# Optimization experiments

Measured on AMD Instinct MI355X. Metric: run time of the kernel, lower is better.

The kernel has to match this reference:

```python
import jax, jax.numpy as jnp
import numpy as np

B, S, D_IN, D_OUT = 4, 2048, 1024, 1024


def setup_inputs() -> dict:
    key = jax.random.key(0)
    ks = jax.random.split(key, 7)
    s_in = 1.0 / np.sqrt(D_IN)
    return {
        "x": jax.random.normal(ks[0], (B, S, D_IN), dtype=jnp.float32),
        "Wq": jax.random.uniform(ks[1], (D_IN, D_OUT), jnp.float32, -s_in, s_in),
        "bq": jax.random.uniform(ks[2], (D_OUT,), jnp.float32, -s_in, s_in),
        "Wk": jax.random.uniform(ks[3], (D_IN, D_OUT), jnp.float32, -s_in, s_in),
        "bk": jax.random.uniform(ks[4], (D_OUT,), jnp.float32, -s_in, s_in),
        "Wv": jax.random.uniform(ks[5], (D_IN, D_OUT), jnp.float32, -s_in, s_in),
        "bv": jax.random.uniform(ks[6], (D_OUT,), jnp.float32, -s_in, s_in),
    }


def reference(x, Wq, bq, Wk, bk, Wv, bv):
    # q,k,v: [B, S, D_OUT]
    q = jnp.einsum("bsd,de->bse", x, Wq) + bq
    k = jnp.einsum("bsd,de->bse", x, Wk) + bk
    v = jnp.einsum("bsd,de->bse", x, Wv) + bv
    scale = 1.0 / jnp.sqrt(jnp.asarray(q.shape[-1], q.dtype))
    scores = jnp.einsum("bqe,bke->bqk", q, k) * scale  # [B, S, S]
    attn = jax.nn.softmax(scores, axis=-1)
    return jnp.einsum("bqk,bke->bqe", attn, v)
```

## Files before the change

kernel.cpp:

```cpp
#include <hip/hip_runtime.h>
#include <hip/hip_bf16.h>
#include <stdint.h>


#define Bsz 4
#define Ssz 2048
#define Dsz 1024

typedef __attribute__((ext_vector_type(8))) short short8;
typedef __attribute__((ext_vector_type(4))) float floatx4;
typedef const __attribute__((address_space(1))) void* gptr_t;
typedef __attribute__((address_space(3))) void* lptr_t;

__device__ __forceinline__ ushort f32_to_bf16(float f) {
    union { float f; uint32_t u; } c; c.f = f;
    uint32_t u = c.u;
    u += 0x7fffu + ((u >> 16) & 1u);
    return (ushort)(u >> 16);
}

template <bool OUT_BF16>
__device__ __forceinline__ void gemm128(
    int bx, int by,
    const ushort* __restrict__ A, int lda,
    const ushort* __restrict__ Bt, int ldb,
    int K,
    void* __restrict__ Cout, int ldc,
    const float* __restrict__ bias, float alpha)
{
    __shared__ ushort lsA[2][128 * 32];
    __shared__ ushort lsB[2][128 * 32];

    const int tid  = threadIdx.x;
    const int row0 = by * 128;
    const int col0 = bx * 128;

    const int lane = tid & 63;
    const int wave = tid >> 6;
    const int wr   = (wave >> 1) * 64;
    const int wc   = (wave & 1) * 64;
    const int m16  = lane & 15;
    const int quad = lane >> 4;

    floatx4 acc[4][4];
#pragma unroll
    for (int i = 0; i < 4; i++)
#pragma unroll
        for (int j = 0; j < 4; j++) acc[i][j] = (floatx4){0.f, 0.f, 0.f, 0.f};

    const int srow = tid >> 2;
    const int skc  = (tid & 3) ^ ((srow >> 1) & 3);
    const ushort* ga = A  + (size_t)(row0 + srow) * lda + skc * 8;
    const ushort* gb = Bt + (size_t)(col0 + srow) * ldb + skc * 8;

    const int aoff = (quad ^ ((m16 >> 1) & 3)) * 8;

    __builtin_amdgcn_global_load_lds((gptr_t)(ga),                     (lptr_t)(lsA[0] + tid * 8),        16, 0, 0);
    __builtin_amdgcn_global_load_lds((gptr_t)(ga + (size_t)64 * lda), (lptr_t)(lsA[0] + 2048 + tid * 8), 16, 0, 0);
    __builtin_amdgcn_global_load_lds((gptr_t)(gb),                     (lptr_t)(lsB[0] + tid * 8),        16, 0, 0);
    __builtin_amdgcn_global_load_lds((gptr_t)(gb + (size_t)64 * ldb), (lptr_t)(lsB[0] + 2048 + tid * 8), 16, 0, 0);

    for (int k0 = 0; k0 < K; k0 += 32) {
        const int cur = (k0 >> 5) & 1;
        __syncthreads();
        if (k0 + 32 < K) {
            const int nxt = cur ^ 1;
            const int kn = k0 + 32;
            __builtin_amdgcn_global_load_lds((gptr_t)(ga + kn),                     (lptr_t)(lsA[nxt] + tid * 8),        16, 0, 0);
            __builtin_amdgcn_global_load_lds((gptr_t)(ga + kn + (size_t)64 * lda), (lptr_t)(lsA[nxt] + 2048 + tid * 8), 16, 0, 0);
            __builtin_amdgcn_global_load_lds((gptr_t)(gb + kn),                     (lptr_t)(lsB[nxt] + tid * 8),        16, 0, 0);
            __builtin_amdgcn_global_load_lds((gptr_t)(gb + kn + (size_t)64 * ldb), (lptr_t)(lsB[nxt] + 2048 + tid * 8), 16, 0, 0);
        }

        short8 af[4], bfr[4];
#pragma unroll
        for (int mi = 0; mi < 4; mi++)
            af[mi] = *(const short8*)&lsA[cur][(wr + mi * 16 + m16) * 32 + aoff];
#pragma unroll
        for (int ni = 0; ni < 4; ni++)
            bfr[ni] = *(const short8*)&lsB[cur][(wc + ni * 16 + m16) * 32 + aoff];
#pragma unroll
        for (int mi = 0; mi < 4; mi++)
#pragma unroll
            for (int ni = 0; ni < 4; ni++)
                acc[mi][ni] = __builtin_amdgcn_mfma_f32_16x16x32_bf16(af[mi], bfr[ni], acc[mi][ni], 0, 0, 0);
    }

#pragma unroll
    for (int ni = 0; ni < 4; ni++) {
        const int gcol = col0 + wc + ni * 16 + m16;
        const float bv = bias ? bias[gcol] : 0.0f;
#pragma unroll
        for (int mi = 0; mi < 4; mi++) {
            const int grow0 = row0 + wr + mi * 16 + quad * 4;
#pragma unroll
            for (int j = 0; j < 4; j++) {
                float v = (acc[mi][ni][j] + bv) * alpha;
                if (OUT_BF16)
                    ((ushort*)Cout)[(size_t)(grow0 + j) * ldc + gcol] = f32_to_bf16(v);
                else
                    ((float*)Cout)[(size_t)(grow0 + j) * ldc + gcol] = v;
            }
        }
    }
}

__global__ __launch_bounds__(256) void k_cvt_x(const float* __restrict__ x, ushort* __restrict__ xb) {
    int i = (blockIdx.x * 256 + threadIdx.x) * 4;
    float4 v = *(const float4*)(x + i);
    ushort4 o;
    o.x = f32_to_bf16(v.x); o.y = f32_to_bf16(v.y);
    o.z = f32_to_bf16(v.z); o.w = f32_to_bf16(v.w);
    *(ushort4*)(xb + i) = o;
}

__global__ __launch_bounds__(256) void k_wt(const float* __restrict__ Wq, const float* __restrict__ Wk,
                                            const float* __restrict__ Wv, ushort* __restrict__ Wt) {
    __shared__ float tile[32][33];
    const int z = blockIdx.z;
    const float* W = (z == 0) ? Wq : ((z == 1) ? Wk : Wv);
    ushort* out = Wt + (size_t)z * Dsz * Dsz;
    const int kb = blockIdx.y * 32, nb = blockIdx.x * 32;
    const int tx = threadIdx.x, ty = threadIdx.y;
#pragma unroll
    for (int j = 0; j < 32; j += 8)
        tile[ty + j][tx] = W[(size_t)(kb + ty + j) * Dsz + nb + tx];
    __syncthreads();
#pragma unroll
    for (int j = 0; j < 32; j += 8)
        out[(size_t)(nb + ty + j) * Dsz + kb + tx] = f32_to_bf16(tile[tx][ty + j]);
}

__global__ __launch_bounds__(256) void k_qkv(const ushort* __restrict__ xb, const ushort* __restrict__ Wt,
                                             const float* __restrict__ bq, const float* __restrict__ bk,
                                             const float* __restrict__ bv, ushort* __restrict__ QKV) {
    const int z = blockIdx.z;
    const int lin = blockIdx.y * 8 + blockIdx.x;
    const int c = lin & 7, m = lin >> 3;
    const int by = 8 * c + (m & 7);
    const int bx = m >> 3;
    const ushort* Bt = Wt + (size_t)z * Dsz * Dsz;
    const float* bias = (z == 0) ? bq : ((z == 1) ? bk : bv);
    ushort* out = QKV + (size_t)z * (Bsz * Ssz) * Dsz;
    const float alpha = (z == 0) ? 0.03125f : 1.0f;
    gemm128<true>(bx, by, xb, Dsz, Bt, Dsz, Dsz, out, Dsz, bias, alpha);
}

__global__ __launch_bounds__(256) void k_scores(const ushort* __restrict__ QKV, float* __restrict__ scores) {
    const int b = blockIdx.z;
    const int lin = blockIdx.y * 16 + blockIdx.x;
    const int c = lin & 7, m = lin >> 3;
    const int by = 2 * c + (m & 1);
    const int bx = m >> 1;
    const ushort* Q = QKV + (size_t)b * Ssz * Dsz;
    const ushort* Kb = QKV + (size_t)(Bsz + b) * Ssz * Dsz;
    gemm128<false>(bx, by, Q, Dsz, Kb, Dsz, Dsz, scores + (size_t)b * Ssz * Ssz, Ssz, nullptr, 1.0f);
}

__global__ __launch_bounds__(256) void k_softmax(float* __restrict__ scores) {
    const size_t row = blockIdx.x;
    float* rp = scores + row * Ssz;
    const int tid = threadIdx.x;
    float4 v0 = ((const float4*)rp)[tid];
    float4 v1 = ((const float4*)rp)[tid + 256];
    float m = fmaxf(fmaxf(fmaxf(v0.x, v0.y), fmaxf(v0.z, v0.w)),
                    fmaxf(fmaxf(v1.x, v1.y), fmaxf(v1.z, v1.w)));
#pragma unroll
    for (int o = 32; o > 0; o >>= 1) m = fmaxf(m, __shfl_down(m, o, 64));
    __shared__ float redm[4];
    if ((tid & 63) == 0) redm[tid >> 6] = m;
    __syncthreads();
    const float rm = fmaxf(fmaxf(redm[0], redm[1]), fmaxf(redm[2], redm[3]));
    v0.x = __expf(v0.x - rm); v0.y = __expf(v0.y - rm);
    v0.z = __expf(v0.z - rm); v0.w = __expf(v0.w - rm);
    v1.x = __expf(v1.x - rm); v1.y = __expf(v1.y - rm);
    v1.z = __expf(v1.z - rm); v1.w = __expf(v1.w - rm);
    float s = v0.x + v0.y + v0.z + v0.w + v1.x + v1.y + v1.z + v1.w;
#pragma unroll
    for (int o = 32; o > 0; o >>= 1) s += __shfl_down(s, o, 64);
    __shared__ float reds[4];
    if ((tid & 63) == 0) reds[tid >> 6] = s;
    __syncthreads();
    const float inv = 1.0f / (reds[0] + reds[1] + reds[2] + reds[3]);
    ushort4 o0, o1;
    o0.x = f32_to_bf16(v0.x * inv); o0.y = f32_to_bf16(v0.y * inv);
    o0.z = f32_to_bf16(v0.z * inv); o0.w = f32_to_bf16(v0.w * inv);
    o1.x = f32_to_bf16(v1.x * inv); o1.y = f32_to_bf16(v1.y * inv);
    o1.z = f32_to_bf16(v1.z * inv); o1.w = f32_to_bf16(v1.w * inv);
    ((ushort4*)rp)[tid] = o0;
    ((ushort4*)rp)[tid + 256] = o1;
}

__global__ __launch_bounds__(256) void k_vt(const ushort* __restrict__ V, ushort* __restrict__ Vt) {
    __shared__ ushort tile[32][33];
    const int b = blockIdx.z;
    const ushort* Vb = V + (size_t)b * Ssz * Dsz;
    ushort* Vtb = Vt + (size_t)b * Dsz * Ssz;
    const int sb = blockIdx.y * 32, db = blockIdx.x * 32;
    const int tx = threadIdx.x, ty = threadIdx.y;
#pragma unroll
    for (int j = 0; j < 32; j += 8)
        tile[ty + j][tx] = Vb[(size_t)(sb + ty + j) * Dsz + db + tx];
    __syncthreads();
#pragma unroll
    for (int j = 0; j < 32; j += 8)
        Vtb[(size_t)(db + ty + j) * Ssz + sb + tx] = tile[tx][ty + j];
}

__global__ __launch_bounds__(256) void k_pv(const float* __restrict__ scores, const ushort* __restrict__ Vt,
                                            float* __restrict__ out) {
    const int b = blockIdx.z;
    const int lin = blockIdx.y * 8 + blockIdx.x;
    const int c = lin & 7, m = lin >> 3;
    const int by = 2 * c + (m & 1);
    const int bx = m >> 1;
    const ushort* P = (const ushort*)(scores + (size_t)b * Ssz * Ssz);
    const ushort* Bt = Vt + (size_t)b * Dsz * Ssz;
    gemm128<false>(bx, by, P, 2 * Ssz, Bt, Ssz, Ssz, out + (size_t)b * Ssz * Dsz, Dsz, nullptr, 1.0f);
}

extern "C" void kernel_launch(void* const* d_in, const int* in_sizes, int n_in,
                              void* d_out, int out_size, void* d_ws, size_t ws_size,
                              hipStream_t stream) {
    const float* x  = (const float*)d_in[0];
    const float* Wq = (const float*)d_in[1];
    const float* bq = (const float*)d_in[2];
    const float* Wk = (const float*)d_in[3];
    const float* bk = (const float*)d_in[4];
    const float* Wv = (const float*)d_in[5];
    const float* bv = (const float*)d_in[6];
    float* out = (float*)d_out;

    char* ws = (char*)d_ws;
    ushort* xb     = (ushort*)(ws);
    ushort* Wt     = (ushort*)(ws + 16777216);
    ushort* QKV    = (ushort*)(ws + 23068672);
    ushort* Vt     = (ushort*)(ws + 73400320);
    float*  scores = (float*) (ws + 90177536);

    k_cvt_x<<<dim3(Bsz * Ssz * Dsz / (256 * 4)), dim3(256), 0, stream>>>(x, xb);
    k_wt<<<dim3(32, 32, 3), dim3(32, 8), 0, stream>>>(Wq, Wk, Wv, Wt);
    k_qkv<<<dim3(Dsz / 128, Bsz * Ssz / 128, 3), dim3(256), 0, stream>>>(xb, Wt, bq, bk, bv, QKV);
    k_vt<<<dim3(Dsz / 32, Ssz / 32, Bsz), dim3(32, 8), 0, stream>>>(QKV + (size_t)2 * Bsz * Ssz * Dsz, Vt);
    k_scores<<<dim3(Ssz / 128, Ssz / 128, Bsz), dim3(256), 0, stream>>>(QKV, scores);
    k_softmax<<<dim3(Bsz * Ssz), dim3(256), 0, stream>>>(scores);
    k_pv<<<dim3(Dsz / 128, Ssz / 128, Bsz), dim3(256), 0, stream>>>(scores, Vt, out);
}
```

Baseline: 290.2 us.

## Pre-pack B operands in MFMA fragment layout and load directly to registers

```diff
diff --git a/kernel.cpp b/kernel.cpp
--- a/kernel.cpp
+++ b/kernel.cpp
@@ -19,17 +19,16 @@
     return (ushort)(u >> 16);
 }
 
-template <bool OUT_BF16>
+template <int OUT_MODE>
 __device__ __forceinline__ void gemm128(
     int bx, int by,
     const ushort* __restrict__ A, int lda,
-    const ushort* __restrict__ Bt, int ldb,
+    const ushort* __restrict__ Bfrag, int KCHB,
     int K,
     void* __restrict__ Cout, int ldc,
     const float* __restrict__ bias, float alpha)
 {
     __shared__ ushort lsA[2][128 * 32];
-    __shared__ ushort lsB[2][128 * 32];
 
     const int tid  = threadIdx.x;
     const int row0 = by * 128;
@@ -41,6 +40,7 @@
     const int wc   = (wave & 1) * 64;
     const int m16  = lane & 15;
     const int quad = lane >> 4;
+    const int ntile0 = bx * 8 + (wave & 1) * 4;
 
     floatx4 acc[4][4];
 #pragma unroll
@@ -50,41 +50,44 @@
 
     const int srow = tid >> 2;
     const int skc  = (tid & 3) ^ ((srow >> 1) & 3);
-    const ushort* ga = A  + (size_t)(row0 + srow) * lda + skc * 8;
-    const ushort* gb = Bt + (size_t)(col0 + srow) * ldb + skc * 8;
+    const ushort* ga = A + (size_t)(row0 + srow) * lda + skc * 8;
 
     const int aoff = (quad ^ ((m16 >> 1) & 3)) * 8;
+
+#define BPTR(ni, kch) ((const short8*)(Bfrag + (((size_t)(ntile0 + (ni)) * KCHB + (kch)) * 64 + lane) * 8))
+
+    short8 bcur[4], bnxt[4];
+#pragma unroll
+    for (int ni = 0; ni < 4; ni++) bcur[ni] = *BPTR(ni, 0);
 
     __builtin_amdgcn_global_load_lds((gptr_t)(ga),                     (lptr_t)(lsA[0] + tid * 8),        16, 0, 0);
     __builtin_amdgcn_global_load_lds((gptr_t)(ga + (size_t)64 * lda), (lptr_t)(lsA[0] + 2048 + tid * 8), 16, 0, 0);
-    __builtin_amdgcn_global_load_lds((gptr_t)(gb),                     (lptr_t)(lsB[0] + tid * 8),        16, 0, 0);
-    __builtin_amdgcn_global_load_lds((gptr_t)(gb + (size_t)64 * ldb), (lptr_t)(lsB[0] + 2048 + tid * 8), 16, 0, 0);
-
-    for (int k0 = 0; k0 < K; k0 += 32) {
-        const int cur = (k0 >> 5) & 1;
+
+    for (int k0 = 0, kch = 0; k0 < K; k0 += 32, kch++) {
+        const int cur = kch & 1;
         __syncthreads();
         if (k0 + 32 < K) {
             const int nxt = cur ^ 1;
             const int kn = k0 + 32;
             __builtin_amdgcn_global_load_lds((gptr_t)(ga + kn),                     (lptr_t)(lsA[nxt] + tid * 8),        16, 0, 0);
             __builtin_amdgcn_global_load_lds((gptr_t)(ga + kn + (size_t)64 * lda), (lptr_t)(lsA[nxt] + 2048 + tid * 8), 16, 0, 0);
-            __builtin_amdgcn_global_load_lds((gptr_t)(gb + kn),                     (lptr_t)(lsB[nxt] + tid * 8),        16, 0, 0);
-            __builtin_amdgcn_global_load_lds((gptr_t)(gb + kn + (size_t)64 * ldb), (lptr_t)(lsB[nxt] + 2048 + tid * 8), 16, 0, 0);
+#pragma unroll
+            for (int ni = 0; ni < 4; ni++) bnxt[ni] = *BPTR(ni, kch + 1);
         }
 
-        short8 af[4], bfr[4];
+        short8 af[4];
 #pragma unroll
         for (int mi = 0; mi < 4; mi++)
             af[mi] = *(const short8*)&lsA[cur][(wr + mi * 16 + m16) * 32 + aoff];
 #pragma unroll
-        for (int ni = 0; ni < 4; ni++)
-            bfr[ni] = *(const short8*)&lsB[cur][(wc + ni * 16 + m16) * 32 + aoff];
-#pragma unroll
         for (int mi = 0; mi < 4; mi++)
 #pragma unroll
             for (int ni = 0; ni < 4; ni++)
-                acc[mi][ni] = __builtin_amdgcn_mfma_f32_16x16x32_bf16(af[mi], bfr[ni], acc[mi][ni], 0, 0, 0);
-    }
+                acc[mi][ni] = __builtin_amdgcn_mfma_f32_16x16x32_bf16(af[mi], bcur[ni], acc[mi][ni], 0, 0, 0);
+#pragma unroll
+        for (int ni = 0; ni < 4; ni++) bcur[ni] = bnxt[ni];
+    }
+#undef BPTR
 
 #pragma unroll
     for (int ni = 0; ni < 4; ni++) {
@@ -96,10 +99,16 @@
 #pragma unroll
             for (int j = 0; j < 4; j++) {
                 float v = (acc[mi][ni][j] + bv) * alpha;
-                if (OUT_BF16)
+                if (OUT_MODE == 0) {
+                    ((float*)Cout)[(size_t)(grow0 + j) * ldc + gcol] = v;
+                } else if (OUT_MODE == 1) {
                     ((ushort*)Cout)[(size_t)(grow0 + j) * ldc + gcol] = f32_to_bf16(v);
-                else
-                    ((float*)Cout)[(size_t)(grow0 + j) * ldc + gcol] = v;
+                } else {
+                    const int s = (grow0 + j) & (Ssz - 1), e = gcol;
+                    const size_t off = (((size_t)(s >> 4) * 32 + (e >> 5)) * 64
+                                        + ((e >> 3) & 3) * 16 + (s & 15)) * 8 + (e & 7);
+                    ((ushort*)Cout)[off] = f32_to_bf16(v);
+                }
             }
         }
     }
@@ -126,9 +135,14 @@
     for (int j = 0; j < 32; j += 8)
         tile[ty + j][tx] = W[(size_t)(kb + ty + j) * Dsz + nb + tx];
     __syncthreads();
-#pragma unroll
-    for (int j = 0; j < 32; j += 8)
-        out[(size_t)(nb + ty + j) * Dsz + kb + tx] = f32_to_bf16(tile[tx][ty + j]);
+    const int kch = kb >> 5;
+    const int q = tx >> 3, jf = tx & 7;
+#pragma unroll
+    for (int i = 0; i < 4; i++) {
+        const int nl = ty + 8 * i;
+        const int nt = (nb + nl) >> 4, nf = nl & 15;
+        out[(((size_t)nt * 32 + kch) * 64 + q * 16 + nf) * 8 + jf] = f32_to_bf16(tile[tx][nl]);
+    }
 }
 
 __global__ __launch_bounds__(256) void k_qkv(const ushort* __restrict__ xb, const ushort* __restrict__ Wt,
@@ -139,11 +153,16 @@
     const int c = lin & 7, m = lin >> 3;
     const int by = 8 * c + (m & 7);
     const int bx = m >> 3;
-    const ushort* Bt = Wt + (size_t)z * Dsz * Dsz;
+    const ushort* Bf = Wt + (size_t)z * Dsz * Dsz;
     const float* bias = (z == 0) ? bq : ((z == 1) ? bk : bv);
     ushort* out = QKV + (size_t)z * (Bsz * Ssz) * Dsz;
-    const float alpha = (z == 0) ? 0.03125f : 1.0f;
-    gemm128<true>(bx, by, xb, Dsz, Bt, Dsz, Dsz, out, Dsz, bias, alpha);
+    if (z == 0)
+        gemm128<1>(bx, by, xb, Dsz, Bf, 32, Dsz, out, Dsz, bias, 0.03125f);
+    else if (z == 1) {
+        ushort* outb = out + (size_t)(by >> 4) * Ssz * Dsz;
+        gemm128<2>(bx, by, xb, Dsz, Bf, 32, Dsz, outb, Dsz, bias, 1.0f);
+    } else
+        gemm128<1>(bx, by, xb, Dsz, Bf, 32, Dsz, out, Dsz, bias, 1.0f);
 }
 
 __global__ __launch_bounds__(256) void k_scores(const ushort* __restrict__ QKV, float* __restrict__ scores) {
@@ -153,8 +172,8 @@
     const int by = 2 * c + (m & 1);
     const int bx = m >> 1;
     const ushort* Q = QKV + (size_t)b * Ssz * Dsz;
-    const ushort* Kb = QKV + (size_t)(Bsz + b) * Ssz * Dsz;
-    gemm128<false>(bx, by, Q, Dsz, Kb, Dsz, Dsz, scores + (size_t)b * Ssz * Ssz, Ssz, nullptr, 1.0f);
+    const ushort* Kf = QKV + (size_t)(Bsz + b) * Ssz * Dsz;
+    gemm128<0>(bx, by, Q, Dsz, Kf, 32, Dsz, scores + (size_t)b * Ssz * Ssz, Ssz, nullptr, 1.0f);
 }
 
 __global__ __launch_bounds__(256) void k_softmax(float* __restrict__ scores) {
@@ -202,9 +221,14 @@
     for (int j = 0; j < 32; j += 8)
         tile[ty + j][tx] = Vb[(size_t)(sb + ty + j) * Dsz + db + tx];
     __syncthreads();
-#pragma unroll
-    for (int j = 0; j < 32; j += 8)
-        Vtb[(size_t)(db + ty + j) * Ssz + sb + tx] = tile[tx][ty + j];
+    const int kch = sb >> 5;
+    const int q = tx >> 3, jf = tx & 7;
+#pragma unroll
+    for (int i = 0; i < 4; i++) {
+        const int el = ty + 8 * i;
+        const int nt = (db + el) >> 4, nf = el & 15;
+        Vtb[(((size_t)nt * 64 + kch) * 64 + q * 16 + nf) * 8 + jf] = tile[tx][el];
+    }
 }
 
 __global__ __launch_bounds__(256) void k_pv(const float* __restrict__ scores, const ushort* __restrict__ Vt,
@@ -215,8 +239,8 @@
     const int by = 2 * c + (m & 1);
     const int bx = m >> 1;
     const ushort* P = (const ushort*)(scores + (size_t)b * Ssz * Ssz);
-    const ushort* Bt = Vt + (size_t)b * Dsz * Ssz;
-    gemm128<false>(bx, by, P, 2 * Ssz, Bt, Ssz, Ssz, out + (size_t)b * Ssz * Dsz, Dsz, nullptr, 1.0f);
+    const ushort* Bf = Vt + (size_t)b * Dsz * Ssz;
+    gemm128<0>(bx, by, P, 2 * Ssz, Bf, 64, Ssz, out + (size_t)b * Ssz * Dsz, Dsz, nullptr, 1.0f);
 }
 
 extern "C" void kernel_launch(void* const* d_in, const int* in_sizes, int n_in,
```

After: 295.4 us. Within noise of the previous version (+1.8%).

## Fuse Q/K/V projections into one GEMM sharing x tiles and writing transposed V

Applied to the files above, without the earlier changes.

```diff
diff --git a/kernel.cpp b/kernel.cpp
--- a/kernel.cpp
+++ b/kernel.cpp
@@ -17,6 +17,109 @@
     uint32_t u = c.u;
     u += 0x7fffu + ((u >> 16) & 1u);
     return (ushort)(u >> 16);
+}
+
+__global__ __launch_bounds__(256, 2) void k_qkv(
+    const ushort* __restrict__ xb, const ushort* __restrict__ Wt,
+    const float* __restrict__ bq, const float* __restrict__ bk,
+    const float* __restrict__ bv, ushort* __restrict__ QKV,
+    ushort* __restrict__ Vt)
+{
+    __shared__ ushort lsA[2][128 * 32];
+    __shared__ ushort lsB[2][3][128 * 32];
+
+    const int tid  = threadIdx.x;
+    const int bx   = blockIdx.x;
+    const int by   = blockIdx.y;
+    const int row0 = by * 128;
+    const int col0 = bx * 128;
+
+    const int lane = tid & 63;
+    const int wave = tid >> 6;
+    const int wr   = (wave >> 1) * 64;
+    const int wc   = (wave & 1) * 64;
+    const int m16  = lane & 15;
+    const int quad = lane >> 4;
+
+    floatx4 acc[3][4][4];
+#pragma unroll
+    for (int z = 0; z < 3; z++)
+#pragma unroll
+        for (int i = 0; i < 4; i++)
+#pragma unroll
+            for (int j = 0; j < 4; j++) acc[z][i][j] = (floatx4){0.f, 0.f, 0.f, 0.f};
+
+    const int srow = tid >> 2;
+    const int skc  = (tid & 3) ^ ((srow >> 1) & 3);
+    const ushort* ga = xb + (size_t)(row0 + srow) * Dsz + skc * 8;
+    const ushort* gb0 = Wt + (size_t)(col0 + srow) * Dsz + skc * 8;
+
+    const int aoff = (quad ^ ((m16 >> 1) & 3)) * 8;
+
+    __builtin_amdgcn_global_load_lds((gptr_t)(ga),                    (lptr_t)(lsA[0] + tid * 8),        16, 0, 0);
+    __builtin_amdgcn_global_load_lds((gptr_t)(ga + (size_t)64 * Dsz), (lptr_t)(lsA[0] + 2048 + tid * 8), 16, 0, 0);
+#pragma unroll
+    for (int z = 0; z < 3; z++) {
+        const ushort* gb = gb0 + (size_t)z * Dsz * Dsz;
+        __builtin_amdgcn_global_load_lds((gptr_t)(gb),                    (lptr_t)(lsB[0][z] + tid * 8),        16, 0, 0);
+        __builtin_amdgcn_global_load_lds((gptr_t)(gb + (size_t)64 * Dsz), (lptr_t)(lsB[0][z] + 2048 + tid * 8), 16, 0, 0);
+    }
+
+    for (int k0 = 0; k0 < Dsz; k0 += 32) {
+        const int cur = (k0 >> 5) & 1;
+        __syncthreads();
+        if (k0 + 32 < Dsz) {
+            const int nxt = cur ^ 1;
+            const int kn = k0 + 32;
+            __builtin_amdgcn_global_load_lds((gptr_t)(ga + kn),                    (lptr_t)(lsA[nxt] + tid * 8),        16, 0, 0);
+            __builtin_amdgcn_global_load_lds((gptr_t)(ga + kn + (size_t)64 * Dsz), (lptr_t)(lsA[nxt] + 2048 + tid * 8), 16, 0, 0);
+#pragma unroll
+            for (int z = 0; z < 3; z++) {
+                const ushort* gb = gb0 + (size_t)z * Dsz * Dsz + kn;
+                __builtin_amdgcn_global_load_lds((gptr_t)(gb),                    (lptr_t)(lsB[nxt][z] + tid * 8),        16, 0, 0);
+                __builtin_amdgcn_global_load_lds((gptr_t)(gb + (size_t)64 * Dsz), (lptr_t)(lsB[nxt][z] + 2048 + tid * 8), 16, 0, 0);
+            }
+        }
+
+        short8 af[4];
+#pragma unroll
+        for (int mi = 0; mi < 4; mi++)
+            af[mi] = *(const short8*)&lsA[cur][(wr + mi * 16 + m16) * 32 + aoff];
+#pragma unroll
+        for (int z = 0; z < 3; z++) {
+            short8 bfr[4];
+#pragma unroll
+            for (int ni = 0; ni < 4; ni++)
+                bfr[ni] = *(const short8*)&lsB[cur][z][(wc + ni * 16 + m16) * 32 + aoff];
+#pragma unroll
+            for (int mi = 0; mi < 4; mi++)
+#pragma unroll
+                for (int ni = 0; ni < 4; ni++)
+                    acc[z][mi][ni] = __builtin_amdgcn_mfma_f32_16x16x32_bf16(af[mi], bfr[ni], acc[z][mi][ni], 0, 0, 0);
+        }
+    }
+
+#pragma unroll
+    for (int ni = 0; ni < 4; ni++) {
+        const int gcol = col0 + wc + ni * 16 + m16;
+        const float bqv = bq[gcol], bkv = bk[gcol], bvv = bv[gcol];
+#pragma unroll
+        for (int mi = 0; mi < 4; mi++) {
+            const int grow0 = row0 + wr + mi * 16 + quad * 4;
+            ushort4 vpack;
+#pragma unroll
+            for (int j = 0; j < 4; j++) {
+                QKV[(size_t)(grow0 + j) * Dsz + gcol] = f32_to_bf16((acc[0][mi][ni][j] + bqv) * 0.03125f);
+                QKV[(size_t)(Bsz * Ssz) * Dsz + (size_t)(grow0 + j) * Dsz + gcol] = f32_to_bf16(acc[1][mi][ni][j] + bkv);
+                const ushort vv = f32_to_bf16(acc[2][mi][ni][j] + bvv);
+                if (j == 0) vpack.x = vv; else if (j == 1) vpack.y = vv;
+                else if (j == 2) vpack.z = vv; else vpack.w = vv;
+            }
+            const int batch = grow0 >> 11;
+            const int s0 = grow0 & (Ssz - 1);
+            *(ushort4*)&Vt[(size_t)batch * Dsz * Ssz + (size_t)gcol * Ssz + s0] = vpack;
+        }
+    }
 }
 
 template <bool OUT_BF16>
@@ -52,7 +155,6 @@
     const int skc  = (tid & 3) ^ ((srow >> 1) & 3);
     const ushort* ga = A  + (size_t)(row0 + srow) * lda + skc * 8;
     const ushort* gb = Bt + (size_t)(col0 + srow) * ldb + skc * 8;
-
     const int aoff = (quad ^ ((m16 >> 1) & 3)) * 8;
 
     __builtin_amdgcn_global_load_lds((gptr_t)(ga),                     (lptr_t)(lsA[0] + tid * 8),        16, 0, 0);
@@ -129,21 +231,6 @@
 #pragma unroll
     for (int j = 0; j < 32; j += 8)
         out[(size_t)(nb + ty + j) * Dsz + kb + tx] = f32_to_bf16(tile[tx][ty + j]);
-}
-
-__global__ __launch_bounds__(256) void k_qkv(const ushort* __restrict__ xb, const ushort* __restrict__ Wt,
-                                             const float* __restrict__ bq, const float* __restrict__ bk,
-                                             const float* __restrict__ bv, ushort* __restrict__ QKV) {
-    const int z = blockIdx.z;
-    const int lin = blockIdx.y * 8 + blockIdx.x;
-    const int c = lin & 7, m = lin >> 3;
-    const int by = 8 * c + (m & 7);
-    const int bx = m >> 3;
-    const ushort* Bt = Wt + (size_t)z * Dsz * Dsz;
-    const float* bias = (z == 0) ? bq : ((z == 1) ? bk : bv);
-    ushort* out = QKV + (size_t)z * (Bsz * Ssz) * Dsz;
-    const float alpha = (z == 0) ? 0.03125f : 1.0f;
-    gemm128<true>(bx, by, xb, Dsz, Bt, Dsz, Dsz, out, Dsz, bias, alpha);
 }
 
 __global__ __launch_bounds__(256) void k_scores(const ushort* __restrict__ QKV, float* __restrict__ scores) {
@@ -191,22 +278,6 @@
     ((ushort4*)rp)[tid + 256] = o1;
 }
 
-__global__ __launch_bounds__(256) void k_vt(const ushort* __restrict__ V, ushort* __restrict__ Vt) {
-    __shared__ ushort tile[32][33];
-    const int b = blockIdx.z;
-    const ushort* Vb = V + (size_t)b * Ssz * Dsz;
-    ushort* Vtb = Vt + (size_t)b * Dsz * Ssz;
-    const int sb = blockIdx.y * 32, db = blockIdx.x * 32;
-    const int tx = threadIdx.x, ty = threadIdx.y;
-#pragma unroll
-    for (int j = 0; j < 32; j += 8)
-        tile[ty + j][tx] = Vb[(size_t)(sb + ty + j) * Dsz + db + tx];
-    __syncthreads();
-#pragma unroll
-    for (int j = 0; j < 32; j += 8)
-        Vtb[(size_t)(db + ty + j) * Ssz + sb + tx] = tile[tx][ty + j];
-}
-
 __global__ __launch_bounds__(256) void k_pv(const float* __restrict__ scores, const ushort* __restrict__ Vt,
                                             float* __restrict__ out) {
     const int b = blockIdx.z;
@@ -240,8 +311,7 @@
 
     k_cvt_x<<<dim3(Bsz * Ssz * Dsz / (256 * 4)), dim3(256), 0, stream>>>(x, xb);
     k_wt<<<dim3(32, 32, 3), dim3(32, 8), 0, stream>>>(Wq, Wk, Wv, Wt);
-    k_qkv<<<dim3(Dsz / 128, Bsz * Ssz / 128, 3), dim3(256), 0, stream>>>(xb, Wt, bq, bk, bv, QKV);
-    k_vt<<<dim3(Dsz / 32, Ssz / 32, Bsz), dim3(32, 8), 0, stream>>>(QKV + (size_t)2 * Bsz * Ssz * Dsz, Vt);
+    k_qkv<<<dim3(Dsz / 128, Bsz * Ssz / 128), dim3(256), 0, stream>>>(xb, Wt, bq, bk, bv, QKV, Vt);
     k_scores<<<dim3(Ssz / 128, Ssz / 128, Bsz), dim3(256), 0, stream>>>(QKV, scores);
     k_softmax<<<dim3(Bsz * Ssz), dim3(256), 0, stream>>>(scores);
     k_pv<<<dim3(Dsz / 128, Ssz / 128, Bsz), dim3(256), 0, stream>>>(scores, Vt, out);
```

New measurement: 277.5 us. 1.05x faster.
